# Kernel tuning notes

Measured on AMD Instinct MI355X. Metric: run time of the kernel, lower is better.

## Reference

```python
import jax, jax.numpy as jnp
import numpy as np

# Two atom types (e.g. H and O) with per-atom auxiliary basis dims 16 and 48.
N_H, D_H = 40000, 16   # number of H-type atoms, basis functions per H atom
N_O, D_O = 20000, 48   # number of O-type atoms, basis functions per O atom
C = 32                 # channels
EPS = 1e-6


def _psd(key, d):
    # Stand-in for the pyscf per-atom overlap matrix: symmetric PSD.
    a = jax.random.normal(key, (d, d), dtype=jnp.float32)
    return a @ a.T / d + 0.5 * jnp.eye(d, dtype=jnp.float32)


def setup_inputs() -> dict:
    key = jax.random.key(0)
    k1, k2, k3 = jax.random.split(key, 3)
    n_total = N_H * D_H + N_O * D_O  # 1,600,000 basis rows
    x = jax.random.normal(k1, (n_total, C), dtype=jnp.float32)
    S_H = _psd(k2, D_H)
    S_O = _psd(k3, D_O)
    # Index arrays equivalent to the boolean atomic_number_masks: all basis
    # functions of H-type atoms first, then O-type (contiguous per atom).
    idx_H = jnp.arange(N_H * D_H, dtype=jnp.int32)
    idx_O = jnp.arange(N_O * D_O, dtype=jnp.int32) + N_H * D_H
    return {"x": x, "S_H": S_H, "S_O": S_O, "idx_H": idx_H, "idx_O": idx_O}


def _l2_function_norm_atom(y, S):
    # y: [n_atoms, d, C], S: [d, d]
    # norm_{a,c} = sum_{i,j} S_ij * y_{a,i,c} * y_{a,j,c}
    norm = jnp.einsum('ij,aic,ajc->ac', S, y, y)
    norm = jnp.sqrt(norm)[:, None, :]  # [n_atoms, 1, C], matches unsqueeze(1)
    return y / (norm + EPS)


def reference(x, S_H, S_O, idx_H, idx_O):
    # H-type atoms: gather -> per-atom bilinear L2 norm -> scatter back
    y = x[idx_H].reshape(N_H, D_H, C)
    x = x.at[idx_H].set(_l2_function_norm_atom(y, S_H).reshape(-1, C))
    # O-type atoms (reads the updated x, as in the sequential torch loop;
    # index sets are disjoint so order does not change the result)
    y = x[idx_O].reshape(N_O, D_O, C)
    x = x.at[idx_O].set(_l2_function_norm_atom(y, S_O).reshape(-1, C))
    return x
```

## Files before the change

### kernel.cpp

```cpp
#include <hip/hip_runtime.h>
#include <cstdint>
#include <cstddef>

#define NH 40000
#define DH 16
#define NO 20000
#define DO_ 48
#define CH 32

__global__ __launch_bounds__(256) void l2norm_h_kernel(
    const float2* __restrict__ x, float2* __restrict__ out,
    const float* __restrict__ S) {
  const int cp = threadIdx.x & 15;
  const int al = threadIdx.x >> 4;
  const int atom = blockIdx.x * 16 + al;
  const size_t base = (size_t)atom * DH * 16 + (size_t)cp;

  float2 yv[DH];
#pragma unroll
  for (int i = 0; i < DH; ++i) yv[i] = x[base + (size_t)i * 16];

  float ax = 0.f, ay = 0.f;
#pragma unroll
  for (int i = 0; i < DH; ++i) {
    float sx = 0.f, sy = 0.f;
#pragma unroll
    for (int j = 0; j < i; ++j) {
      const float s = S[i * DH + j];
      sx = fmaf(s, yv[j].x, sx);
      sy = fmaf(s, yv[j].y, sy);
    }
    const float sd = S[i * DH + i];
    const float tx = fmaf(sd, yv[i].x, 2.f * sx);
    const float ty = fmaf(sd, yv[i].y, 2.f * sy);
    ax = fmaf(tx, yv[i].x, ax);
    ay = fmaf(ty, yv[i].y, ay);
  }

  const float ix = 1.f / (sqrtf(ax) + 1e-6f);
  const float iy = 1.f / (sqrtf(ay) + 1e-6f);

#pragma unroll
  for (int i = 0; i < DH; ++i)
    out[base + (size_t)i * 16] = make_float2(yv[i].x * ix, yv[i].y * iy);
}

__global__ __launch_bounds__(256) void l2norm_o_kernel(
    const float* __restrict__ x, float* __restrict__ out,
    const float* __restrict__ S) {
  const int c  = threadIdx.x & 31;
  const int al = threadIdx.x >> 5;
  const int atom = blockIdx.x * 8 + al;
  const size_t base = (size_t)NH * DH * CH + (size_t)atom * DO_ * CH + (size_t)c;

  float yv[DO_];
#pragma unroll
  for (int i = 0; i < DO_; ++i) yv[i] = x[base + (size_t)i * CH];

  float acc = 0.f;
#pragma unroll
  for (int i = 0; i < DO_; ++i) {
    float s = 0.f;
#pragma unroll
    for (int j = 0; j < i; ++j)
      s = fmaf(S[i * DO_ + j], yv[j], s);
    const float t = fmaf(S[i * DO_ + i], yv[i], 2.f * s);
    acc = fmaf(t, yv[i], acc);
  }

  const float inv = 1.f / (sqrtf(acc) + 1e-6f);
#pragma unroll
  for (int i = 0; i < DO_; ++i) out[base + (size_t)i * CH] = yv[i] * inv;
}

extern "C" void kernel_launch(void* const* d_in, const int* in_sizes, int n_in,
                              void* d_out, int out_size, void* d_ws, size_t ws_size,
                              hipStream_t stream) {
  const float* x  = (const float*)d_in[0];
  const float* SH = (const float*)d_in[1];
  const float* SO = (const float*)d_in[2];
  float* out = (float*)d_out;

  l2norm_o_kernel<<<NO / 8, 256, 0, stream>>>(x, out, SO);
  l2norm_h_kernel<<<NH / 16, 256, 0, stream>>>((const float2*)x,
                                               (float2*)out, SH);
}
```

Baseline: 361.7 us.

## Fuse H and O normalization kernels into one interleaved launch with nontemporal stores

Merges the two per-atom-type kernels into a single launch whose even blocks handle O atoms and odd blocks handle H atoms (2500 each). This removes one kernel launch and the tail/gap between the two kernels, and lets memory-heavy work from both types overlap on the device. Output stores become nontemporal to avoid polluting cache with write-once data. Register pressure of the fused kernel is set by the larger O path, which may lower occupancy for the H blocks.

Result: faster. 352.9 us (-2.4%).

```diff
diff --git a/kernel.cpp b/kernel.cpp
--- a/kernel.cpp
+++ b/kernel.cpp
@@ -8,69 +8,83 @@
 #define DO_ 48
 #define CH 32
 
-__global__ __launch_bounds__(256) void l2norm_h_kernel(
-    const float2* __restrict__ x, float2* __restrict__ out,
-    const float* __restrict__ S) {
-  const int cp = threadIdx.x & 15;
-  const int al = threadIdx.x >> 4;
-  const int atom = blockIdx.x * 16 + al;
-  const size_t base = (size_t)atom * DH * 16 + (size_t)cp;
+#define OBLOCKS (NO / 8)
+#define HBLOCKS (NH / 16)
 
-  float2 yv[DH];
+typedef float f32x2 __attribute__((ext_vector_type(2)));
+
+__global__ __launch_bounds__(256) void l2norm_fused(
+    const float* __restrict__ x, float* __restrict__ out,
+    const float* __restrict__ SH, const float* __restrict__ SO) {
+  const int b = blockIdx.x;
+  const int idx = b >> 1;
+
+  if ((b & 1) == 0) {
+    const int c  = threadIdx.x & 31;
+    const int al = threadIdx.x >> 5;
+    const int atom = idx * 8 + al;
+    const size_t base =
+        (size_t)NH * DH * CH + (size_t)atom * DO_ * CH + (size_t)c;
+
+    float yv[DO_];
 #pragma unroll
-  for (int i = 0; i < DH; ++i) yv[i] = x[base + (size_t)i * 16];
+    for (int i = 0; i < DO_; ++i) yv[i] = x[base + (size_t)i * CH];
 
-  float ax = 0.f, ay = 0.f;
+    float acc = 0.f;
 #pragma unroll
-  for (int i = 0; i < DH; ++i) {
-    float sx = 0.f, sy = 0.f;
+    for (int i = 0; i < DO_; ++i) {
+      float s = 0.f;
 #pragma unroll
-    for (int j = 0; j < i; ++j) {
-      const float s = S[i * DH + j];
-      sx = fmaf(s, yv[j].x, sx);
-      sy = fmaf(s, yv[j].y, sy);
+      for (int j = 0; j < i; ++j)
+        s = fmaf(SO[i * DO_ + j], yv[j], s);
+      const float t = fmaf(SO[i * DO_ + i], yv[i], 2.f * s);
+      acc = fmaf(t, yv[i], acc);
     }
-    const float sd = S[i * DH + i];
-    const float tx = fmaf(sd, yv[i].x, 2.f * sx);
-    const float ty = fmaf(sd, yv[i].y, 2.f * sy);
-    ax = fmaf(tx, yv[i].x, ax);
-    ay = fmaf(ty, yv[i].y, ay);
-  }
 
-  const float ix = 1.f / (sqrtf(ax) + 1e-6f);
-  const float iy = 1.f / (sqrtf(ay) + 1e-6f);
+    const float inv = 1.f / (sqrtf(acc) + 1e-6f);
+#pragma unroll
+    for (int i = 0; i < DO_; ++i)
+      __builtin_nontemporal_store(yv[i] * inv, &out[base + (size_t)i * CH]);
+  } else {
+    const f32x2* __restrict__ x2 = (const f32x2*)x;
+    f32x2* __restrict__ o2 = (f32x2*)out;
+    const int cp = threadIdx.x & 15;
+    const int al = threadIdx.x >> 4;
+    const int atom = idx * 16 + al;
+    const size_t base = (size_t)atom * DH * 16 + (size_t)cp;
+
+    f32x2 yv[DH];
+#pragma unroll
+    for (int i = 0; i < DH; ++i) yv[i] = x2[base + (size_t)i * 16];
+
+    float ax = 0.f, ay = 0.f;
+#pragma unroll
+    for (int i = 0; i < DH; ++i) {
+      float sx = 0.f, sy = 0.f;
+#pragma unroll
+      for (int j = 0; j < i; ++j) {
+        const float s = SH[i * DH + j];
+        sx = fmaf(s, yv[j].x, sx);
+        sy = fmaf(s, yv[j].y, sy);
+      }
+      const float sd = SH[i * DH + i];
+      const float tx = fmaf(sd, yv[i].x, 2.f * sx);
+      const float ty = fmaf(sd, yv[i].y, 2.f * sy);
+      ax = fmaf(tx, yv[i].x, ax);
+      ay = fmaf(ty, yv[i].y, ay);
+    }
+
+    const float ix = 1.f / (sqrtf(ax) + 1e-6f);
+    const float iy = 1.f / (sqrtf(ay) + 1e-6f);
 
 #pragma unroll
-  for (int i = 0; i < DH; ++i)
-    out[base + (size_t)i * 16] = make_float2(yv[i].x * ix, yv[i].y * iy);
-}
-
-__global__ __launch_bounds__(256) void l2norm_o_kernel(
-    const float* __restrict__ x, float* __restrict__ out,
-    const float* __restrict__ S) {
-  const int c  = threadIdx.x & 31;
-  const int al = threadIdx.x >> 5;
-  const int atom = blockIdx.x * 8 + al;
-  const size_t base = (size_t)NH * DH * CH + (size_t)atom * DO_ * CH + (size_t)c;
-
-  float yv[DO_];
-#pragma unroll
-  for (int i = 0; i < DO_; ++i) yv[i] = x[base + (size_t)i * CH];
-
-  float acc = 0.f;
-#pragma unroll
-  for (int i = 0; i < DO_; ++i) {
-    float s = 0.f;
-#pragma unroll
-    for (int j = 0; j < i; ++j)
-      s = fmaf(S[i * DO_ + j], yv[j], s);
-    const float t = fmaf(S[i * DO_ + i], yv[i], 2.f * s);
-    acc = fmaf(t, yv[i], acc);
+    for (int i = 0; i < DH; ++i) {
+      f32x2 r;
+      r.x = yv[i].x * ix;
+      r.y = yv[i].y * iy;
+      __builtin_nontemporal_store(r, &o2[base + (size_t)i * 16]);
+    }
   }
-
-  const float inv = 1.f / (sqrtf(acc) + 1e-6f);
-#pragma unroll
-  for (int i = 0; i < DO_; ++i) out[base + (size_t)i * CH] = yv[i] * inv;
 }
 
 extern "C" void kernel_launch(void* const* d_in, const int* in_sizes, int n_in,
@@ -81,7 +95,5 @@
   const float* SO = (const float*)d_in[2];
   float* out = (float*)d_out;
 
-  l2norm_o_kernel<<<NO / 8, 256, 0, stream>>>(x, out, SO);
-  l2norm_h_kernel<<<NH / 16, 256, 0, stream>>>((const float2*)x,
-                                               (float2*)out, SH);
+  l2norm_fused<<<OBLOCKS + HBLOCKS, 256, 0, stream>>>(x, out, SH, SO);
 }
```

## Fuse H and O normalization into one kernel with float4 channel vectors

Applied to the files above, without the earlier changes.

Merges the two per-atom-type kernels into a single launch that interleaves one O-atom block with two H-atom blocks by block index. Each thread now handles four channels with 128-bit vector loads and stores instead of one or two. This removes one kernel launch and the tail between the two launches, and widens memory transactions. In exchange, the O path keeps 48 float4 values live per thread, which raises register pressure and may lower occupancy.

Result: slower. 377.9 us (+4.5%).

```diff
diff --git a/kernel.cpp b/kernel.cpp
--- a/kernel.cpp
+++ b/kernel.cpp
@@ -8,69 +8,75 @@
 #define DO_ 48
 #define CH 32
 
-__global__ __launch_bounds__(256) void l2norm_h_kernel(
-    const float2* __restrict__ x, float2* __restrict__ out,
-    const float* __restrict__ S) {
-  const int cp = threadIdx.x & 15;
-  const int al = threadIdx.x >> 4;
-  const int atom = blockIdx.x * 16 + al;
-  const size_t base = (size_t)atom * DH * 16 + (size_t)cp;
+typedef float f32x4 __attribute__((ext_vector_type(4)));
 
-  float2 yv[DH];
+#define XO_BASE4 ((size_t)NH * DH * CH / 4)
+#define OBLOCKS (NO / 32)
+#define HBLOCKS (NH / 32)
+
+__global__ __launch_bounds__(256) void l2norm_fused(
+    const f32x4* __restrict__ x4, f32x4* __restrict__ o4,
+    const float* __restrict__ SH, const float* __restrict__ SO) {
+  const int b = blockIdx.x;
+  const int q  = threadIdx.x & 7;
+  const int al = threadIdx.x >> 3;
+
+  if (b % 3 == 0) {
+    const int atom = (b / 3) * 32 + al;
+    const size_t base = XO_BASE4 + (size_t)atom * (DO_ * 8) + (size_t)q;
+
+    f32x4 yv[DO_];
 #pragma unroll
-  for (int i = 0; i < DH; ++i) yv[i] = x[base + (size_t)i * 16];
+    for (int i = 0; i < DO_; ++i) yv[i] = x4[base + (size_t)i * 8];
 
-  float ax = 0.f, ay = 0.f;
+    f32x4 acc = {0.f, 0.f, 0.f, 0.f};
 #pragma unroll
-  for (int i = 0; i < DH; ++i) {
-    float sx = 0.f, sy = 0.f;
+    for (int i = 0; i < DO_; ++i) {
+      f32x4 s = {0.f, 0.f, 0.f, 0.f};
 #pragma unroll
-    for (int j = 0; j < i; ++j) {
-      const float s = S[i * DH + j];
-      sx = fmaf(s, yv[j].x, sx);
-      sy = fmaf(s, yv[j].y, sy);
+      for (int j = 0; j < i; ++j)
+        s += SO[i * DO_ + j] * yv[j];
+      acc += (SO[i * DO_ + i] * yv[i] + 2.f * s) * yv[i];
     }
-    const float sd = S[i * DH + i];
-    const float tx = fmaf(sd, yv[i].x, 2.f * sx);
-    const float ty = fmaf(sd, yv[i].y, 2.f * sy);
-    ax = fmaf(tx, yv[i].x, ax);
-    ay = fmaf(ty, yv[i].y, ay);
-  }
 
-  const float ix = 1.f / (sqrtf(ax) + 1e-6f);
-  const float iy = 1.f / (sqrtf(ay) + 1e-6f);
+    f32x4 inv;
+    inv.x = 1.f / (sqrtf(acc.x) + 1e-6f);
+    inv.y = 1.f / (sqrtf(acc.y) + 1e-6f);
+    inv.z = 1.f / (sqrtf(acc.z) + 1e-6f);
+    inv.w = 1.f / (sqrtf(acc.w) + 1e-6f);
 
 #pragma unroll
-  for (int i = 0; i < DH; ++i)
-    out[base + (size_t)i * 16] = make_float2(yv[i].x * ix, yv[i].y * iy);
-}
+    for (int i = 0; i < DO_; ++i)
+      o4[base + (size_t)i * 8] = yv[i] * inv;
+  } else {
+    const int idx = (b / 3) * 2 + (b % 3 - 1);
+    const int atom = idx * 32 + al;
+    const size_t base = (size_t)atom * (DH * 8) + (size_t)q;
 
-__global__ __launch_bounds__(256) void l2norm_o_kernel(
-    const float* __restrict__ x, float* __restrict__ out,
-    const float* __restrict__ S) {
-  const int c  = threadIdx.x & 31;
-  const int al = threadIdx.x >> 5;
-  const int atom = blockIdx.x * 8 + al;
-  const size_t base = (size_t)NH * DH * CH + (size_t)atom * DO_ * CH + (size_t)c;
+    f32x4 yv[DH];
+#pragma unroll
+    for (int i = 0; i < DH; ++i) yv[i] = x4[base + (size_t)i * 8];
 
-  float yv[DO_];
+    f32x4 acc = {0.f, 0.f, 0.f, 0.f};
 #pragma unroll
-  for (int i = 0; i < DO_; ++i) yv[i] = x[base + (size_t)i * CH];
+    for (int i = 0; i < DH; ++i) {
+      f32x4 s = {0.f, 0.f, 0.f, 0.f};
+#pragma unroll
+      for (int j = 0; j < i; ++j)
+        s += SH[i * DH + j] * yv[j];
+      acc += (SH[i * DH + i] * yv[i] + 2.f * s) * yv[i];
+    }
 
-  float acc = 0.f;
+    f32x4 inv;
+    inv.x = 1.f / (sqrtf(acc.x) + 1e-6f);
+    inv.y = 1.f / (sqrtf(acc.y) + 1e-6f);
+    inv.z = 1.f / (sqrtf(acc.z) + 1e-6f);
+    inv.w = 1.f / (sqrtf(acc.w) + 1e-6f);
+
 #pragma unroll
-  for (int i = 0; i < DO_; ++i) {
-    float s = 0.f;
-#pragma unroll
-    for (int j = 0; j < i; ++j)
-      s = fmaf(S[i * DO_ + j], yv[j], s);
-    const float t = fmaf(S[i * DO_ + i], yv[i], 2.f * s);
-    acc = fmaf(t, yv[i], acc);
+    for (int i = 0; i < DH; ++i)
+      o4[base + (size_t)i * 8] = yv[i] * inv;
   }
-
-  const float inv = 1.f / (sqrtf(acc) + 1e-6f);
-#pragma unroll
-  for (int i = 0; i < DO_; ++i) out[base + (size_t)i * CH] = yv[i] * inv;
 }
 
 extern "C" void kernel_launch(void* const* d_in, const int* in_sizes, int n_in,
@@ -81,7 +87,6 @@
   const float* SO = (const float*)d_in[2];
   float* out = (float*)d_out;
 
-  l2norm_o_kernel<<<NO / 8, 256, 0, stream>>>(x, out, SO);
-  l2norm_h_kernel<<<NH / 16, 256, 0, stream>>>((const float2*)x,
-                                               (float2*)out, SH);
+  l2norm_fused<<<OBLOCKS + HBLOCKS, 256, 0, stream>>>(
+      (const f32x4*)x, (f32x4*)out, SH, SO);
 }
```
